# Kernel tuning notes

Measured on AMD Instinct MI355X. Metric: run time of the kernel, lower is better.

## Reference

```python
import jax, jax.numpy as jnp
import numpy as np

N, E, D, L = 100000, 1_600_000, 128, 8


def setup_inputs() -> dict:
    key = jax.random.key(0)
    k0, k1, k2 = jax.random.split(key, 3)
    x = jax.random.normal(k0, (N, D), dtype=jnp.float32)
    edge_index = jax.random.randint(k1, (2, E), 0, N, dtype=jnp.int64)
    Ws = jax.random.normal(k2, (L, D, D), dtype=jnp.float32) / np.float32(np.sqrt(D))
    bs = jnp.zeros((L, D), dtype=jnp.float32)
    return {"x": x, "edge_index": edge_index, "Ws": Ws, "bs": bs}


def _gcn_conv(h, W, b, src, dst, norm_edge, self_norm):
    """PyG GCNConv: linear -> sym-normalized aggregate (with self loops) -> +bias."""
    h = h @ W                                    # [N, D]
    msg = h[src] * norm_edge[:, None]            # [E, D] gather + scale
    agg = jax.ops.segment_sum(msg, dst, num_segments=h.shape[0])  # scatter-add
    return agg + h * self_norm[:, None] + b      # self-loop term fused in


def reference(x, edge_index, Ws, bs):
    src, dst = edge_index[0], edge_index[1]
    # degree of (A + I) on target nodes, symmetric normalization
    deg = jax.ops.segment_sum(jnp.ones((src.shape[0],), jnp.float32), dst,
                              num_segments=x.shape[0]) + 1.0
    dis = deg ** -0.5                            # deg >= 1, safe
    norm_edge = dis[src] * dis[dst]              # per-edge norm
    self_norm = dis * dis                        # per-node self-loop norm

    n_layers = Ws.shape[0]
    h = x
    initial = x
    for i in range(n_layers):
        h = _gcn_conv(h, Ws[i], bs[i], src, dst, norm_edge, self_norm)
        if i > 0:
            h = h + initial
            initial = h
        h = jax.nn.relu(h)
        if i < n_layers - 1:
            # NOTE: at i == 0 the original indexes layers[-1] (last layer) — faithful.
            j = i - 1
            h = h + _gcn_conv(h, Ws[j], bs[j], src, dst, norm_edge, self_norm)
    return h
```

## Files before the change

kernel.cpp:

```cpp
#include <hip/hip_runtime.h>

#define D 128
#define SCAN_CH 1024
#define SA_STRIDE 136
#define SC_STRIDE 132

typedef _Float16 f16x8 __attribute__((ext_vector_type(8)));
typedef float f32x4 __attribute__((ext_vector_type(4)));


__global__ void hist_kernel(const int* __restrict__ dst, int* __restrict__ counts, int E) {
  int stride = gridDim.x * blockDim.x;
  for (int e = blockIdx.x * blockDim.x + threadIdx.x; e < E; e += stride)
    atomicAdd(&counts[dst[e]], 1);
}

__global__ void dis_kernel(const int* __restrict__ counts, float* __restrict__ dis, int N) {
  int n = blockIdx.x * blockDim.x + threadIdx.x;
  if (n < N) dis[n] = rsqrtf((float)counts[n] + 1.0f);
}

__global__ __launch_bounds__(256) void scan_phaseA(const int* __restrict__ counts,
    int* __restrict__ blksum, int N) {
  __shared__ int red[256];
  int base = blockIdx.x * SCAN_CH;
  int t = threadIdx.x;
  int s = 0;
  #pragma unroll
  for (int j = 0; j < 4; ++j) {
    int idx = base + t * 4 + j;
    if (idx < N) s += counts[idx];
  }
  red[t] = s;
  __syncthreads();
  for (int d = 128; d > 0; d >>= 1) {
    if (t < d) red[t] += red[t + d];
    __syncthreads();
  }
  if (t == 0) blksum[blockIdx.x] = red[0];
}

__global__ __launch_bounds__(1024) void scan_phaseB(int* __restrict__ blksum, int NB) {
  __shared__ int sa[1024], sb[1024];
  int t = threadIdx.x;
  int v = (t < NB) ? blksum[t] : 0;
  sa[t] = v;
  __syncthreads();
  int* a = sa; int* b = sb;
  for (int d = 1; d < 1024; d <<= 1) {
    int val = a[t] + ((t >= d) ? a[t - d] : 0);
    b[t] = val;
    __syncthreads();
    int* tmp = a; a = b; b = tmp;
  }
  if (t < NB) blksum[t] = a[t] - v;
}

__global__ __launch_bounds__(256) void scan_phaseC(const int* __restrict__ counts,
    const int* __restrict__ blksum, int* __restrict__ row_ptr, int* __restrict__ fillp, int N) {
  __shared__ int ra[256], rb[256];
  int base = blockIdx.x * SCAN_CH;
  int t = threadIdx.x;
  int v[4]; int s = 0;
  #pragma unroll
  for (int j = 0; j < 4; ++j) {
    int idx = base + t * 4 + j;
    v[j] = (idx < N) ? counts[idx] : 0;
    s += v[j];
  }
  ra[t] = s;
  __syncthreads();
  int* a = ra; int* b = rb;
  for (int d = 1; d < 256; d <<= 1) {
    int val = a[t] + ((t >= d) ? a[t - d] : 0);
    b[t] = val;
    __syncthreads();
    int* tmp = a; a = b; b = tmp;
  }
  int excl = a[t] - s + blksum[blockIdx.x];
  #pragma unroll
  for (int j = 0; j < 4; ++j) {
    int idx = base + t * 4 + j;
    if (idx < N) {
      row_ptr[idx] = excl;
      fillp[idx] = excl;
      excl += v[j];
      if (idx == N - 1) row_ptr[N] = excl;
    }
  }
}

__global__ void fill_kernel(const int* __restrict__ src, const int* __restrict__ dst,
    int* __restrict__ fillp, int* __restrict__ csr_src, int E) {
  int stride = gridDim.x * blockDim.x;
  for (int e = blockIdx.x * blockDim.x + threadIdx.x; e < E; e += stride) {
    int s = src[e], d = dst[e];
    int p = atomicAdd(&fillp[d], 1);
    csr_src[p] = s;
  }
}


__global__ void conv_x_kernel(const float* __restrict__ x, const float* __restrict__ dis,
    _Float16* __restrict__ hs, int total8) {
  int i = blockIdx.x * blockDim.x + threadIdx.x;
  if (i >= total8) return;
  int node = i >> 4;
  float dn = dis[node];
  const float4* p = (const float4*)(x + (size_t)i * 8);
  float4 a = p[0], b = p[1];
  f16x8 v;
  v[0] = (_Float16)(dn * a.x); v[1] = (_Float16)(dn * a.y);
  v[2] = (_Float16)(dn * a.z); v[3] = (_Float16)(dn * a.w);
  v[4] = (_Float16)(dn * b.x); v[5] = (_Float16)(dn * b.y);
  v[6] = (_Float16)(dn * b.z); v[7] = (_Float16)(dn * b.w);
  *(f16x8*)(hs + (size_t)i * 8) = v;
}

__global__ void repack_w_kernel(const float* __restrict__ Ws, _Float16* __restrict__ Wf, int total) {
  int t = blockIdx.x * blockDim.x + threadIdx.x;
  if (t >= total) return;
  int lane = t & 63;
  int nb = (t >> 6) & 7;
  int kb = (t >> 9) & 3;
  int l = t >> 11;
  int col = nb * 16 + (lane & 15);
  int k0 = kb * 32 + (lane >> 4) * 8;
  const float* w = Ws + (size_t)l * D * D;
  f16x8 v;
  #pragma unroll
  for (int j = 0; j < 8; ++j) v[j] = (_Float16)w[(k0 + j) * D + col];
  *(f16x8*)(Wf + (size_t)t * 8) = v;
}

__global__ __launch_bounds__(256) void conv_fused_kernel(
    const _Float16* __restrict__ hs, const int* __restrict__ row_ptr,
    const int* __restrict__ csr_src, const float* __restrict__ dis,
    const f16x8* __restrict__ Wf, const float* __restrict__ bias,
    const float* __restrict__ init_in, float* __restrict__ init_out,
    float* __restrict__ out, _Float16* __restrict__ hs_out, int N, int flags) {
  __shared__ _Float16 sA[16 * SA_STRIDE];
  __shared__ float sC[16 * SC_STRIDE];
  int tid = threadIdx.x;
  int node0 = blockIdx.x * 16;
  int ng = tid >> 4;
  int li = tid & 15;
  int n = node0 + ng;

  {
    float acc[8];
    #pragma unroll
    for (int j = 0; j < 8; ++j) acc[j] = 0.f;
    f16x8 g = {};
    if (n < N) {
      int beg = row_ptr[n], end = row_ptr[n + 1];
      int c0 = li * 8;
      #pragma unroll 4
      for (int e = beg; e < end; ++e) {
        int s = csr_src[e];
        f16x8 v = *(const f16x8*)&hs[(size_t)s * D + c0];
        #pragma unroll
        for (int j = 0; j < 8; ++j) acc[j] += (float)v[j];
      }
      f16x8 own = *(const f16x8*)&hs[(size_t)n * D + c0];
      float dn = dis[n];
      #pragma unroll
      for (int j = 0; j < 8; ++j) g[j] = (_Float16)(dn * (acc[j] + (float)own[j]));
    }
    *(f16x8*)&sA[ng * SA_STRIDE + li * 8] = g;
  }

  int wave = tid >> 6, lane = tid & 63;
  f16x8 bf[4][2];
  #pragma unroll
  for (int kb = 0; kb < 4; ++kb)
    #pragma unroll
    for (int i = 0; i < 2; ++i)
      bf[kb][i] = Wf[(kb * 8 + wave * 2 + i) * 64 + lane];
  __syncthreads();

  f32x4 ca = {0.f, 0.f, 0.f, 0.f}, cb = {0.f, 0.f, 0.f, 0.f};
  #pragma unroll
  for (int kb = 0; kb < 4; ++kb) {
    f16x8 a = *(const f16x8*)&sA[(lane & 15) * SA_STRIDE + kb * 32 + (lane >> 4) * 8];
    ca = __builtin_amdgcn_mfma_f32_16x16x32_f16(a, bf[kb][0], ca, 0, 0, 0);
    cb = __builtin_amdgcn_mfma_f32_16x16x32_f16(a, bf[kb][1], cb, 0, 0, 0);
  }

  {
    int colb = wave * 32 + (lane & 15);
    int rowb = (lane >> 4) * 4;
    #pragma unroll
    for (int r = 0; r < 4; ++r) {
      sC[(rowb + r) * SC_STRIDE + colb]      = ca[r];
      sC[(rowb + r) * SC_STRIDE + colb + 16] = cb[r];
    }
  }
  __syncthreads();

  if (n >= N) return;
  {
    int c0 = li * 8;
    float v[8];
    float4 s0 = *(const float4*)&sC[ng * SC_STRIDE + c0];
    float4 s1 = *(const float4*)&sC[ng * SC_STRIDE + c0 + 4];
    float4 b0 = *(const float4*)&bias[c0];
    float4 b1 = *(const float4*)&bias[c0 + 4];
    v[0] = s0.x + b0.x; v[1] = s0.y + b0.y; v[2] = s0.z + b0.z; v[3] = s0.w + b0.w;
    v[4] = s1.x + b1.x; v[5] = s1.y + b1.y; v[6] = s1.z + b1.z; v[7] = s1.w + b1.w;
    size_t off = (size_t)n * D + c0;
    if (flags & 1) {
      float4 i0 = *(const float4*)&init_in[off];
      float4 i1 = *(const float4*)&init_in[off + 4];
      v[0] += i0.x; v[1] += i0.y; v[2] += i0.z; v[3] += i0.w;
      v[4] += i1.x; v[5] += i1.y; v[6] += i1.z; v[7] += i1.w;
    }
    if (flags & 2) {
      *(float4*)&init_out[off]     = make_float4(v[0], v[1], v[2], v[3]);
      *(float4*)&init_out[off + 4] = make_float4(v[4], v[5], v[6], v[7]);
    }
    if (flags & 4) {
      #pragma unroll
      for (int j = 0; j < 8; ++j) v[j] = fmaxf(v[j], 0.f);
    }
    if (flags & 8) {
      float4 p0 = *(const float4*)&out[off];
      float4 p1 = *(const float4*)&out[off + 4];
      v[0] += p0.x; v[1] += p0.y; v[2] += p0.z; v[3] += p0.w;
      v[4] += p1.x; v[5] += p1.y; v[6] += p1.z; v[7] += p1.w;
    }
    *(float4*)&out[off]     = make_float4(v[0], v[1], v[2], v[3]);
    *(float4*)&out[off + 4] = make_float4(v[4], v[5], v[6], v[7]);
    if (flags & 16) {
      float dn = dis[n];
      f16x8 h8;
      #pragma unroll
      for (int j = 0; j < 8; ++j) h8[j] = (_Float16)(dn * v[j]);
      *(f16x8*)&hs_out[off] = h8;
    }
  }
}


extern "C" void kernel_launch(void* const* d_in, const int* in_sizes, int n_in,
                              void* d_out, int out_size, void* d_ws, size_t ws_size,
                              hipStream_t stream) {
  const float* x = (const float*)d_in[0];
  const int* ei = (const int*)d_in[1];
  const float* Ws = (const float*)d_in[2];
  const float* bs = (const float*)d_in[3];
  float* out = (float*)d_out;

  const int N = in_sizes[0] / D;
  const int E = in_sizes[1] / 2;
  const int L = in_sizes[2] / (D * D);
  const int* src = ei;
  const int* dst = ei + E;

  uintptr_t p = (uintptr_t)d_ws;
  auto alloc = [&](size_t bytes) {
    uintptr_t r = p;
    p = (r + bytes + 255) & ~(uintptr_t)255;
    return r;
  };
  float*     dis      = (float*)alloc((size_t)N * 4);
  int*       counts   = (int*)  alloc((size_t)N * 4);
  int*       row_ptr  = (int*)  alloc((size_t)(N + 1) * 4);
  int*       fillp    = (int*)  alloc((size_t)N * 4);
  int*       blksum   = (int*)  alloc((size_t)1024 * 4);
  int*       csr_src  = (int*)  alloc((size_t)E * 4);
  _Float16*  hs_a     = (_Float16*)alloc((size_t)N * D * 2);
  _Float16*  hs_b     = (_Float16*)alloc((size_t)N * D * 2);
  float*     init_buf = (float*)alloc((size_t)N * D * 4);
  _Float16*  Wf       = (_Float16*)alloc((size_t)L * 4 * 8 * 64 * 8 * 2);

  const int NB = (N + SCAN_CH - 1) / SCAN_CH;

  hipMemsetAsync(counts, 0, (size_t)N * 4, stream);
  hist_kernel<<<1024, 256, 0, stream>>>(dst, counts, E);
  dis_kernel<<<(N + 255) / 256, 256, 0, stream>>>(counts, dis, N);
  scan_phaseA<<<NB, 256, 0, stream>>>(counts, blksum, N);
  scan_phaseB<<<1, 1024, 0, stream>>>(blksum, NB);
  scan_phaseC<<<NB, 256, 0, stream>>>(counts, blksum, row_ptr, fillp, N);
  fill_kernel<<<1024, 256, 0, stream>>>(src, dst, fillp, csr_src, E);
  conv_x_kernel<<<(N * 16 + 255) / 256, 256, 0, stream>>>(x, dis, hs_a, N * 16);
  {
    int total = L * 2048;
    repack_w_kernel<<<(total + 255) / 256, 256, 0, stream>>>(Ws, Wf, total);
  }

  const int conv_grid = (N + 15) / 16;
  _Float16* hsp[2] = {hs_a, hs_b};
  int cur = 0;

  for (int i = 0; i < L; ++i) {
    int flags;
    if (i == 0)          flags = 4 | 16;
    else if (i == L - 1) flags = 1 | 4;
    else                 flags = 1 | 2 | 4 | 16;
    const float* init_in = (i <= 1) ? x : (const float*)init_buf;
    conv_fused_kernel<<<conv_grid, 256, 0, stream>>>(hsp[cur], row_ptr, csr_src, dis,
        (const f16x8*)(Wf + (size_t)i * 2048 * 8), bs + (size_t)i * D,
        init_in, init_buf, out, hsp[cur ^ 1], N, flags);
    if (flags & 16) cur ^= 1;
    if (i < L - 1) {
      int j = (i == 0) ? (L - 1) : (i - 1);
      conv_fused_kernel<<<conv_grid, 256, 0, stream>>>(hsp[cur], row_ptr, csr_src, dis,
          (const f16x8*)(Wf + (size_t)j * 2048 * 8), bs + (size_t)j * D,
          nullptr, nullptr, out, hsp[cur ^ 1], N, 8 | 16);
      cur ^= 1;
    }
  }
}
```

Baseline: 1.397 ms.

## Process 64 nodes per block in conv kernel and partition atomics by node range

The fused conv kernel now handles 64 nodes per block instead of 16. The weight fragments loaded into registers are reused across four MFMA row tiles, and shared memory for the A and C staging buffers is aliased behind an extra barrier. The histogram and CSR fill kernels split blocks into 8 destination ranges, so each block's atomics land on a smaller contiguous slice of counters, which is meant to improve L2 locality. The cost is that every block now reads the full dst array, 8x the index reads, and the conv grid has fewer blocks, which lowers parallelism for the latency-bound gather.

Measured after the change: 1.443 ms. 3.3% more time.

```diff
diff --git a/kernel.cpp b/kernel.cpp
--- a/kernel.cpp
+++ b/kernel.cpp
@@ -4,15 +4,38 @@
 #define SCAN_CH 1024
 #define SA_STRIDE 136
 #define SC_STRIDE 132
+#define NPB 64
 
 typedef _Float16 f16x8 __attribute__((ext_vector_type(8)));
 typedef float f32x4 __attribute__((ext_vector_type(4)));
 
 
-__global__ void hist_kernel(const int* __restrict__ dst, int* __restrict__ counts, int E) {
-  int stride = gridDim.x * blockDim.x;
-  for (int e = blockIdx.x * blockDim.x + threadIdx.x; e < E; e += stride)
-    atomicAdd(&counts[dst[e]], 1);
+__global__ void hist_kernel(const int* __restrict__ dst, int* __restrict__ counts,
+                            int E, int N) {
+  int range = blockIdx.x & 7;
+  int lo = (int)(((long long)N * range) >> 3);
+  int hi = (int)(((long long)N * (range + 1)) >> 3);
+  int stride = (gridDim.x >> 3) * blockDim.x;
+  for (int e = (blockIdx.x >> 3) * blockDim.x + threadIdx.x; e < E; e += stride) {
+    int d = dst[e];
+    if (d >= lo && d < hi) atomicAdd(&counts[d], 1);
+  }
+}
+
+__global__ void fill_kernel(const int* __restrict__ src, const int* __restrict__ dst,
+    int* __restrict__ fillp, int* __restrict__ csr_src, int E, int N) {
+  int range = blockIdx.x & 7;
+  int lo = (int)(((long long)N * range) >> 3);
+  int hi = (int)(((long long)N * (range + 1)) >> 3);
+  int stride = (gridDim.x >> 3) * blockDim.x;
+  for (int e = (blockIdx.x >> 3) * blockDim.x + threadIdx.x; e < E; e += stride) {
+    int d = dst[e];
+    if (d >= lo && d < hi) {
+      int s = src[e];
+      int p = atomicAdd(&fillp[d], 1);
+      csr_src[p] = s;
+    }
+  }
 }
 
 __global__ void dis_kernel(const int* __restrict__ counts, float* __restrict__ dis, int N) {
@@ -87,16 +110,6 @@
       excl += v[j];
       if (idx == N - 1) row_ptr[N] = excl;
     }
-  }
-}
-
-__global__ void fill_kernel(const int* __restrict__ src, const int* __restrict__ dst,
-    int* __restrict__ fillp, int* __restrict__ csr_src, int E) {
-  int stride = gridDim.x * blockDim.x;
-  for (int e = blockIdx.x * blockDim.x + threadIdx.x; e < E; e += stride) {
-    int s = src[e], d = dst[e];
-    int p = atomicAdd(&fillp[d], 1);
-    csr_src[p] = s;
   }
 }
 
@@ -139,22 +152,25 @@
     const f16x8* __restrict__ Wf, const float* __restrict__ bias,
     const float* __restrict__ init_in, float* __restrict__ init_out,
     float* __restrict__ out, _Float16* __restrict__ hs_out, int N, int flags) {
-  __shared__ _Float16 sA[16 * SA_STRIDE];
-  __shared__ float sC[16 * SC_STRIDE];
+  __shared__ __align__(16) char smem[NPB * SC_STRIDE * 4];
+  _Float16* sA = (_Float16*)smem;
+  float* sC = (float*)smem;
   int tid = threadIdx.x;
-  int node0 = blockIdx.x * 16;
+  int node0 = blockIdx.x * NPB;
   int ng = tid >> 4;
   int li = tid & 15;
-  int n = node0 + ng;
-
-  {
-    float acc[8];
-    #pragma unroll
-    for (int j = 0; j < 8; ++j) acc[j] = 0.f;
+  int c0 = li * 8;
+
+  #pragma unroll
+  for (int k = 0; k < 4; ++k) {
+    int lr = ng + 16 * k;
+    int n = node0 + lr;
     f16x8 g = {};
     if (n < N) {
+      float acc[8];
+      #pragma unroll
+      for (int j = 0; j < 8; ++j) acc[j] = 0.f;
       int beg = row_ptr[n], end = row_ptr[n + 1];
-      int c0 = li * 8;
       #pragma unroll 4
       for (int e = beg; e < end; ++e) {
         int s = csr_src[e];
@@ -167,7 +183,7 @@
       #pragma unroll
       for (int j = 0; j < 8; ++j) g[j] = (_Float16)(dn * (acc[j] + (float)own[j]));
     }
-    *(f16x8*)&sA[ng * SA_STRIDE + li * 8] = g;
+    *(f16x8*)&sA[lr * SA_STRIDE + c0] = g;
   }
 
   int wave = tid >> 6, lane = tid & 63;
@@ -179,33 +195,43 @@
       bf[kb][i] = Wf[(kb * 8 + wave * 2 + i) * 64 + lane];
   __syncthreads();
 
-  f32x4 ca = {0.f, 0.f, 0.f, 0.f}, cb = {0.f, 0.f, 0.f, 0.f};
-  #pragma unroll
-  for (int kb = 0; kb < 4; ++kb) {
-    f16x8 a = *(const f16x8*)&sA[(lane & 15) * SA_STRIDE + kb * 32 + (lane >> 4) * 8];
-    ca = __builtin_amdgcn_mfma_f32_16x16x32_f16(a, bf[kb][0], ca, 0, 0, 0);
-    cb = __builtin_amdgcn_mfma_f32_16x16x32_f16(a, bf[kb][1], cb, 0, 0, 0);
-  }
+  f32x4 ca[4], cb[4];
+  #pragma unroll
+  for (int rt = 0; rt < 4; ++rt) { ca[rt] = (f32x4){0,0,0,0}; cb[rt] = (f32x4){0,0,0,0}; }
+  #pragma unroll
+  for (int rt = 0; rt < 4; ++rt) {
+    #pragma unroll
+    for (int kb = 0; kb < 4; ++kb) {
+      f16x8 a = *(const f16x8*)&sA[(rt * 16 + (lane & 15)) * SA_STRIDE + kb * 32 + (lane >> 4) * 8];
+      ca[rt] = __builtin_amdgcn_mfma_f32_16x16x32_f16(a, bf[kb][0], ca[rt], 0, 0, 0);
+      cb[rt] = __builtin_amdgcn_mfma_f32_16x16x32_f16(a, bf[kb][1], cb[rt], 0, 0, 0);
+    }
+  }
+  __syncthreads();
 
   {
     int colb = wave * 32 + (lane & 15);
     int rowb = (lane >> 4) * 4;
     #pragma unroll
-    for (int r = 0; r < 4; ++r) {
-      sC[(rowb + r) * SC_STRIDE + colb]      = ca[r];
-      sC[(rowb + r) * SC_STRIDE + colb + 16] = cb[r];
-    }
-  }
-  __syncthreads();
-
-  if (n >= N) return;
-  {
-    int c0 = li * 8;
+    for (int rt = 0; rt < 4; ++rt)
+      #pragma unroll
+      for (int r = 0; r < 4; ++r) {
+        sC[(rt * 16 + rowb + r) * SC_STRIDE + colb]      = ca[rt][r];
+        sC[(rt * 16 + rowb + r) * SC_STRIDE + colb + 16] = cb[rt][r];
+      }
+  }
+  __syncthreads();
+
+  float4 b0 = *(const float4*)&bias[c0];
+  float4 b1 = *(const float4*)&bias[c0 + 4];
+  #pragma unroll
+  for (int k = 0; k < 4; ++k) {
+    int lr = ng + 16 * k;
+    int n = node0 + lr;
+    if (n >= N) continue;
     float v[8];
-    float4 s0 = *(const float4*)&sC[ng * SC_STRIDE + c0];
-    float4 s1 = *(const float4*)&sC[ng * SC_STRIDE + c0 + 4];
-    float4 b0 = *(const float4*)&bias[c0];
-    float4 b1 = *(const float4*)&bias[c0 + 4];
+    float4 s0 = *(const float4*)&sC[lr * SC_STRIDE + c0];
+    float4 s1 = *(const float4*)&sC[lr * SC_STRIDE + c0 + 4];
     v[0] = s0.x + b0.x; v[1] = s0.y + b0.y; v[2] = s0.z + b0.z; v[3] = s0.w + b0.w;
     v[4] = s1.x + b1.x; v[5] = s1.y + b1.y; v[6] = s1.z + b1.z; v[7] = s1.w + b1.w;
     size_t off = (size_t)n * D + c0;
@@ -277,19 +303,19 @@
   const int NB = (N + SCAN_CH - 1) / SCAN_CH;
 
   hipMemsetAsync(counts, 0, (size_t)N * 4, stream);
-  hist_kernel<<<1024, 256, 0, stream>>>(dst, counts, E);
+  hist_kernel<<<8 * 192, 256, 0, stream>>>(dst, counts, E, N);
   dis_kernel<<<(N + 255) / 256, 256, 0, stream>>>(counts, dis, N);
   scan_phaseA<<<NB, 256, 0, stream>>>(counts, blksum, N);
   scan_phaseB<<<1, 1024, 0, stream>>>(blksum, NB);
   scan_phaseC<<<NB, 256, 0, stream>>>(counts, blksum, row_ptr, fillp, N);
-  fill_kernel<<<1024, 256, 0, stream>>>(src, dst, fillp, csr_src, E);
+  fill_kernel<<<8 * 192, 256, 0, stream>>>(src, dst, fillp, csr_src, E, N);
   conv_x_kernel<<<(N * 16 + 255) / 256, 256, 0, stream>>>(x, dis, hs_a, N * 16);
   {
     int total = L * 2048;
     repack_w_kernel<<<(total + 255) / 256, 256, 0, stream>>>(Ws, Wf, total);
   }
 
-  const int conv_grid = (N + 15) / 16;
+  const int conv_grid = (N + NPB - 1) / NPB;
   _Float16* hsp[2] = {hs_a, hs_b};
   int cur = 0;
 
```
